# Optimization experiments

Measured on AMD Instinct MI355X. Metric: run time of the kernel, lower is better.

Reference implementation:

```python
import jax, jax.numpy as jnp
import numpy as np

NUM_ENT = 50000
NUM_REL2 = 474   # num_relations * 2
E = 400000
D = 100          # embedding / hidden dim (hardcoded in module)
B = 4            # num_bases
NEG_SLOPE = 0.2  # PyG RGATConv default


def setup_inputs() -> dict:
    key = jax.random.key(0)
    ks = jax.random.split(key, 8)
    inp = {
        "entity": jnp.arange(NUM_ENT, dtype=jnp.int32),
        "edge_index": jax.random.randint(ks[0], (2, E), 0, NUM_ENT),
        "edge_type": jax.random.randint(ks[1], (E,), 0, NUM_REL2),
        "edge_norm": jax.random.normal(ks[2], (E,), dtype=jnp.float32),
        "emb": jax.random.normal(ks[3], (NUM_ENT, D), dtype=jnp.float32),
    }
    scale = 1.0 / np.sqrt(D).astype(np.float32)
    for i, p in enumerate(("1", "2")):
        k = jax.random.split(ks[4 + i], 4)
        inp["basis" + p] = jax.random.normal(k[0], (B, D, D), dtype=jnp.float32) * scale
        inp["att" + p] = jax.random.normal(k[1], (NUM_REL2, B), dtype=jnp.float32) * 0.5
        inp["q" + p] = jax.random.normal(k[2], (D, 1), dtype=jnp.float32) * scale
        inp["k" + p] = jax.random.normal(k[3], (D, 1), dtype=jnp.float32) * scale
        inp["bias" + p] = jnp.zeros((D,), jnp.float32)
    return inp


def segment_softmax(scores, seg, num_segments):
    # numerically stable softmax over edges grouped by destination node
    m = jax.ops.segment_max(scores, seg, num_segments=num_segments)
    ex = jnp.exp(scores - m[seg])
    s = jax.ops.segment_sum(ex, seg, num_segments=num_segments)
    return ex / (s[seg] + 1e-16)


def rgat_conv(x, src, dst, etype, basis, att, q, k, bias, num_nodes):
    # basis decomposition: per-relation weight W_r = sum_b att[r,b] * basis[b]
    # computed implicitly: project x through each basis once, mix per-edge.
    xb = jnp.einsum('ni,bio->nbo', x, basis)          # [N, B, D]
    att_e = att[etype]                                # [E, B]
    hj = jnp.einsum('eb,ebo->eo', att_e, xb[src])     # transformed source feats [E, D]
    xq = jnp.einsum('nbo,oh->nb', xb, q)              # per-node, per-basis q-score [N, B]
    xk = jnp.einsum('nbo,oh->nb', xb, k)
    q_e = jnp.sum(att_e * xq[dst], axis=1)            # [E]
    k_e = jnp.sum(att_e * xk[src], axis=1)            # [E]
    alpha = jax.nn.leaky_relu(q_e + k_e, NEG_SLOPE)   # additive self-attention
    alpha = segment_softmax(alpha, dst, num_nodes)    # across-relation softmax per dst
    out = jax.ops.segment_sum(alpha[:, None] * hj, dst, num_segments=num_nodes)
    return out + bias


def reference(entity, edge_index, edge_type, edge_norm, emb,
              basis1, att1, q1, k1, bias1,
              basis2, att2, q2, k2, bias2):
    src, dst = edge_index[0], edge_index[1]
    n = entity.shape[0]
    x = emb[entity]                                   # [N, 100]
    x = jax.nn.relu(rgat_conv(x, src, dst, edge_type, basis1, att1, q1, k1, bias1, n))
    # dropout is identity in eval mode
    x = rgat_conv(x, src, dst, edge_type, basis2, att2, q2, k2, bias2, n)
    return x
```

## Files before the change

### kernel.cpp

```cpp
#include <hip/hip_runtime.h>

constexpr int N = 50000;
constexpr int E = 400000;
constexpr int D = 100;
constexpr int B = 4;
constexpr float NEG_SLOPE = 0.2f;

constexpr int SCAN_CHUNK = 2048;
constexpr int NB_SCAN = (N + SCAN_CHUNK - 1) / SCAN_CHUNK;
constexpr int CAP = 128;


__global__ void k_hist(const int* __restrict__ dst, int* __restrict__ deg) {
  int i = blockIdx.x * blockDim.x + threadIdx.x;
  int stride = gridDim.x * blockDim.x;
  for (; i < E; i += stride) atomicAdd(&deg[dst[i]], 1);
}

__global__ void k_scan1(const int* __restrict__ deg, int* __restrict__ incl,
                        int* __restrict__ bsums) {
  __shared__ int lds[256];
  int tid = threadIdx.x;
  int base = blockIdx.x * SCAN_CHUNK + tid * 8;
  int v[8]; int s = 0;
#pragma unroll
  for (int j = 0; j < 8; ++j) {
    int idx = base + j;
    int x = (idx < N) ? deg[idx] : 0;
    v[j] = x; s += x;
  }
  lds[tid] = s; __syncthreads();
  for (int off = 1; off < 256; off <<= 1) {
    int t = (tid >= off) ? lds[tid - off] : 0;
    __syncthreads();
    lds[tid] += t;
    __syncthreads();
  }
  int run = lds[tid] - s;
#pragma unroll
  for (int j = 0; j < 8; ++j) {
    int idx = base + j;
    run += v[j];
    if (idx < N) incl[idx] = run;
  }
  if (tid == 255) bsums[blockIdx.x] = lds[255];
}

__global__ void k_scan2(int* __restrict__ bsums, int nb) {
  if (threadIdx.x == 0 && blockIdx.x == 0) {
    int run = 0;
    for (int i = 0; i < nb; ++i) { int t = bsums[i]; bsums[i] = run; run += t; }
  }
}

__global__ void k_scan3(const int* __restrict__ incl, const int* __restrict__ bsums,
                        int* __restrict__ offs) {
  int i = blockIdx.x * blockDim.x + threadIdx.x;
  int stride = gridDim.x * blockDim.x;
  for (; i < N; i += stride) {
    offs[i + 1] = incl[i] + bsums[i / SCAN_CHUNK];
    if (i == 0) offs[0] = 0;
  }
}

__global__ void k_scatter(const int* __restrict__ srcArr, const int* __restrict__ dst,
                          const int* __restrict__ etype, const int* __restrict__ offs,
                          int* __restrict__ cursor, int* __restrict__ ssorted,
                          int* __restrict__ esorted) {
  int i = blockIdx.x * blockDim.x + threadIdx.x;
  int stride = gridDim.x * blockDim.x;
  for (; i < E; i += stride) {
    int d = dst[i];
    int pos = offs[d] + atomicAdd(&cursor[d], 1);
    ssorted[pos] = srcArr[i];
    esorted[pos] = etype[i];
  }
}

__global__ void k_gather(const float* __restrict__ emb, const int* __restrict__ entity,
                         float* __restrict__ X) {
  int idx = blockIdx.x * blockDim.x + threadIdx.x;
  int total = N * (D / 4);
  int stride = gridDim.x * blockDim.x;
  for (; idx < total; idx += stride) {
    int n = idx / (D / 4), c = idx % (D / 4);
    int r = entity[n];
    *(float4*)(X + (size_t)n * D + c * 4) = *(const float4*)(emb + (size_t)r * D + c * 4);
  }
}


__global__ void k_qbkb(const float* __restrict__ basis, const float* __restrict__ qv,
                       const float* __restrict__ kv, float* __restrict__ qb,
                       float* __restrict__ kb) {
  int t = blockIdx.x * blockDim.x + threadIdx.x;
  if (t < B * D) {
    const float* row = basis + t * D;
    float sq = 0.f, sk = 0.f;
    for (int o = 0; o < D; ++o) { float r = row[o]; sq += r * qv[o]; sk += r * kv[o]; }
    qb[t] = sq; kb[t] = sk;
  }
}

__global__ __launch_bounds__(256) void k_xqxk(
    const float* __restrict__ X, const float* __restrict__ qb,
    const float* __restrict__ kb, float* __restrict__ xq, float* __restrict__ xk) {
  __shared__ float qb_s[B * D], kb_s[B * D];
  int tid = threadIdx.x;
  for (int i = tid; i < B * D; i += 256) { qb_s[i] = qb[i]; kb_s[i] = kb[i]; }
  __syncthreads();
  int n = blockIdx.x * 256 + tid;
  if (n >= N) return;
  const float* x = X + (size_t)n * D;
  float aq[B] = {}, ak[B] = {};
  for (int i = 0; i < D; i += 4) {
    float4 xv = *(const float4*)(x + i);
#pragma unroll
    for (int b = 0; b < B; ++b) {
      float4 qv = *(const float4*)&qb_s[b * D + i];
      float4 kv = *(const float4*)&kb_s[b * D + i];
      aq[b] += xv.x * qv.x + xv.y * qv.y + xv.z * qv.z + xv.w * qv.w;
      ak[b] += xv.x * kv.x + xv.y * kv.y + xv.z * kv.z + xv.w * kv.w;
    }
  }
  *(float4*)(xq + (size_t)n * 4) = make_float4(aq[0], aq[1], aq[2], aq[3]);
  *(float4*)(xk + (size_t)n * 4) = make_float4(ak[0], ak[1], ak[2], ak[3]);
}

__device__ __forceinline__ float edge_score_p(int s, int et,
                                              const float* __restrict__ att,
                                              const float4 xq4,
                                              const float* __restrict__ xk,
                                              float4* a_out) {
  float4 a = *(const float4*)(att + et * 4);
  float4 xs = *(const float4*)(xk + s * 4);
  float qe = a.x * xq4.x + a.y * xq4.y + a.z * xq4.z + a.w * xq4.w;
  float ke = a.x * xs.x + a.y * xs.y + a.z * xs.z + a.w * xs.w;
  float sc = qe + ke;
  *a_out = a;
  return sc >= 0.f ? sc : NEG_SLOPE * sc;
}

__global__ __launch_bounds__(128) void k_node(
    const float* __restrict__ feat, const int* __restrict__ ssorted,
    const int* __restrict__ esorted, const float* __restrict__ att,
    const float* __restrict__ xq, const float* __restrict__ xk,
    const int* __restrict__ offs, float* __restrict__ agg) {
  int n = blockIdx.x;
  int tid = threadIdx.x;
  int lane = tid & 63, wid = tid >> 6;
  int o0 = offs[n], o1 = offs[n + 1];
  int deg = o1 - o0;
  float4 xq4 = *(const float4*)(xq + (size_t)n * 4);
  __shared__ float red[2];
  __shared__ float sc[CAP];
  __shared__ float4 a4[CAP];
  __shared__ int sbuf[CAP];

  if (deg <= CAP) {
    for (int i = tid; i < deg; i += 128) {
      int s = ssorted[o0 + i];
      int et = esorted[o0 + i];
      float4 a;
      float v = edge_score_p(s, et, att, xq4, xk, &a);
      sc[i] = v; a4[i] = a; sbuf[i] = s;
    }
    __syncthreads();
    float lm = -3.4e38f;
    for (int i = tid; i < deg; i += 128) lm = fmaxf(lm, sc[i]);
#pragma unroll
    for (int off = 32; off >= 1; off >>= 1) lm = fmaxf(lm, __shfl_xor(lm, off));
    if (lane == 0) red[wid] = lm;
    __syncthreads();
    float m = fmaxf(red[0], red[1]);
    __syncthreads();
    float ls = 0.f;
    for (int i = tid; i < deg; i += 128) {
      float ex = __expf(sc[i] - m);
      sc[i] = ex;
      ls += ex;
    }
#pragma unroll
    for (int off = 32; off >= 1; off >>= 1) ls += __shfl_xor(ls, off);
    if (lane == 0) red[wid] = ls;
    __syncthreads();
    float inv = 1.f / (red[0] + red[1] + 1e-16f);
    for (int i = tid; i < deg; i += 128) {
      float p = sc[i] * inv;
      float4 a = a4[i];
      a.x *= p; a.y *= p; a.z *= p; a.w *= p;
      a4[i] = a;
    }
    __syncthreads();
    if (tid < D) {
      float acc0 = 0.f, acc1 = 0.f, acc2 = 0.f, acc3 = 0.f;
      int i = 0;
      for (; i + 1 < deg; i += 2) {
        float4 aA = a4[i];     int sA = sbuf[i];
        float4 aB = a4[i + 1]; int sB = sbuf[i + 1];
        float xA = feat[(size_t)sA * D + tid];
        float xB = feat[(size_t)sB * D + tid];
        acc0 += aA.x * xA + aB.x * xB;
        acc1 += aA.y * xA + aB.y * xB;
        acc2 += aA.z * xA + aB.z * xB;
        acc3 += aA.w * xA + aB.w * xB;
      }
      if (i < deg) {
        float4 a = a4[i]; int s = sbuf[i];
        float xv = feat[(size_t)s * D + tid];
        acc0 += a.x * xv; acc1 += a.y * xv; acc2 += a.z * xv; acc3 += a.w * xv;
      }
      float* ag = agg + (size_t)n * (B * D) + tid;
      ag[0 * D] = acc0; ag[1 * D] = acc1; ag[2 * D] = acc2; ag[3 * D] = acc3;
    }
  } else {
    float lm = -3.4e38f;
    for (int i = tid; i < deg; i += 128) {
      float4 a;
      lm = fmaxf(lm, edge_score_p(ssorted[o0 + i], esorted[o0 + i], att, xq4, xk, &a));
    }
#pragma unroll
    for (int off = 32; off >= 1; off >>= 1) lm = fmaxf(lm, __shfl_xor(lm, off));
    if (lane == 0) red[wid] = lm;
    __syncthreads();
    float m = fmaxf(red[0], red[1]);
    __syncthreads();
    float ls = 0.f;
    for (int i = tid; i < deg; i += 128) {
      float4 a;
      ls += __expf(edge_score_p(ssorted[o0 + i], esorted[o0 + i], att, xq4, xk, &a) - m);
    }
#pragma unroll
    for (int off = 32; off >= 1; off >>= 1) ls += __shfl_xor(ls, off);
    if (lane == 0) red[wid] = ls;
    __syncthreads();
    float inv = 1.f / (red[0] + red[1] + 1e-16f);
    if (tid < D) {
      float acc0 = 0.f, acc1 = 0.f, acc2 = 0.f, acc3 = 0.f;
      for (int i = 0; i < deg; ++i) {
        int s = ssorted[o0 + i];
        float4 a;
        float v = edge_score_p(s, esorted[o0 + i], att, xq4, xk, &a);
        float p = __expf(v - m) * inv;
        float xv = feat[(size_t)s * D + tid];
        acc0 += p * a.x * xv;
        acc1 += p * a.y * xv;
        acc2 += p * a.z * xv;
        acc3 += p * a.w * xv;
      }
      float* ag = agg + (size_t)n * (B * D) + tid;
      ag[0 * D] = acc0; ag[1 * D] = acc1; ag[2 * D] = acc2; ag[3 * D] = acc3;
    }
  }
}

template <bool RELU>
__global__ __launch_bounds__(256) void k_gemm(const float* __restrict__ A,
                                              const float* __restrict__ W,
                                              const float* __restrict__ bias,
                                              float* __restrict__ out) {
  __shared__ float A_lds[64][36];
  __shared__ float W_lds[32][128];
  int tid = threadIdx.x;
  int nblk = blockIdx.x * 64;
  int o_lo = (tid & 15) * 4;
  int n_base = (tid >> 4) * 4;
  float acc[4][8] = {};
  for (int kc = 0; kc < 400; kc += 32) {
#pragma unroll
    for (int j = 0; j < 2; ++j) {
      int idx = tid + j * 256;
      int n_l = idx >> 3;
      int k4 = (idx & 7) * 4;
      int gn = nblk + n_l;
      float4 av = make_float4(0.f, 0.f, 0.f, 0.f);
      if (gn < N && kc + k4 + 3 < 400) av = *(const float4*)(A + (size_t)gn * 400 + kc + k4);
      *(float4*)&A_lds[n_l][k4] = av;
    }
#pragma unroll
    for (int j = 0; j < 4; ++j) {
      int idx = tid + j * 256;
      int k = idx >> 5;
      int o4 = (idx & 31) * 4;
      float4 v = make_float4(0.f, 0.f, 0.f, 0.f);
      if (o4 < D && kc + k < 400) v = *(const float4*)(W + (size_t)(kc + k) * D + o4);
      *(float4*)&W_lds[k][o4] = v;
    }
    __syncthreads();
#pragma unroll 4
    for (int k = 0; k < 32; ++k) {
      float4 w0 = *(const float4*)&W_lds[k][o_lo];
      float4 w1 = *(const float4*)&W_lds[k][o_lo + 64];
      float w[8] = {w0.x, w0.y, w0.z, w0.w, w1.x, w1.y, w1.z, w1.w};
#pragma unroll
      for (int i = 0; i < 4; ++i) {
        float a = A_lds[n_base + i][k];
#pragma unroll
        for (int jj = 0; jj < 8; ++jj) acc[i][jj] += a * w[jj];
      }
    }
    __syncthreads();
  }
  bool hi_ok = (o_lo + 64 < D - 3);
  float4 b0 = *(const float4*)(bias + o_lo);
  float4 b1 = hi_ok ? *(const float4*)(bias + o_lo + 64) : make_float4(0, 0, 0, 0);
#pragma unroll
  for (int i = 0; i < 4; ++i) {
    int gn = nblk + n_base + i;
    if (gn < N) {
      float4 r0, r1;
      r0.x = acc[i][0] + b0.x; r0.y = acc[i][1] + b0.y;
      r0.z = acc[i][2] + b0.z; r0.w = acc[i][3] + b0.w;
      r1.x = acc[i][4] + b1.x; r1.y = acc[i][5] + b1.y;
      r1.z = acc[i][6] + b1.z; r1.w = acc[i][7] + b1.w;
      if (RELU) {
        r0.x = fmaxf(r0.x, 0.f); r0.y = fmaxf(r0.y, 0.f);
        r0.z = fmaxf(r0.z, 0.f); r0.w = fmaxf(r0.w, 0.f);
        r1.x = fmaxf(r1.x, 0.f); r1.y = fmaxf(r1.y, 0.f);
        r1.z = fmaxf(r1.z, 0.f); r1.w = fmaxf(r1.w, 0.f);
      }
      *(float4*)(out + (size_t)gn * D + o_lo) = r0;
      if (hi_ok) *(float4*)(out + (size_t)gn * D + o_lo + 64) = r1;
    }
  }
}


extern "C" void kernel_launch(void* const* d_in, const int* in_sizes, int n_in,
                              void* d_out, int out_size, void* d_ws, size_t ws_size,
                              hipStream_t stream) {
  const int* entity = (const int*)d_in[0];
  const int* edge_index = (const int*)d_in[1];
  const int* etype = (const int*)d_in[2];
  const float* emb = (const float*)d_in[4];
  const float* basis1 = (const float*)d_in[5];
  const float* att1 = (const float*)d_in[6];
  const float* q1 = (const float*)d_in[7];
  const float* k1 = (const float*)d_in[8];
  const float* bias1 = (const float*)d_in[9];
  const float* basis2 = (const float*)d_in[10];
  const float* att2 = (const float*)d_in[11];
  const float* q2 = (const float*)d_in[12];
  const float* k2 = (const float*)d_in[13];
  const float* bias2 = (const float*)d_in[14];
  float* out = (float*)d_out;

  const int* srcArr = edge_index;
  const int* dstArr = edge_index + E;

  float* ws = (float*)d_ws;
  float* agg = ws;
  float* X1 = agg + (size_t)N * B * D;
  float* xq = X1 + (size_t)N * D;
  float* xk = xq + (size_t)N * B;
  float* qb = xk + (size_t)N * B;
  float* kb = qb + B * D;
  int* ssorted = (int*)(kb + B * D);
  int* esorted = ssorted + E;
  int* offs = esorted + E;
  int* deg = offs + (N + 1);
  int* cursor = deg + N;
  int* incl = cursor + N;
  int* bsums = incl + N;

  hipMemsetAsync(deg, 0, N * sizeof(int), stream);
  hipMemsetAsync(cursor, 0, N * sizeof(int), stream);
  k_hist<<<512, 256, 0, stream>>>(dstArr, deg);
  k_scan1<<<NB_SCAN, 256, 0, stream>>>(deg, incl, bsums);
  k_scan2<<<1, 64, 0, stream>>>(bsums, NB_SCAN);
  k_scan3<<<256, 256, 0, stream>>>(incl, bsums, offs);
  k_scatter<<<512, 256, 0, stream>>>(srcArr, dstArr, etype, offs, cursor, ssorted, esorted);
  k_gather<<<1024, 256, 0, stream>>>(emb, entity, X1);

  k_qbkb<<<2, 256, 0, stream>>>(basis1, q1, k1, qb, kb);
  k_xqxk<<<(N + 255) / 256, 256, 0, stream>>>(X1, qb, kb, xq, xk);
  k_node<<<N, 128, 0, stream>>>(X1, ssorted, esorted, att1, xq, xk, offs, agg);
  k_gemm<true><<<(N + 63) / 64, 256, 0, stream>>>(agg, basis1, bias1, out);

  k_qbkb<<<2, 256, 0, stream>>>(basis2, q2, k2, qb, kb);
  k_xqxk<<<(N + 255) / 256, 256, 0, stream>>>(out, qb, kb, xq, xk);
  k_node<<<N, 128, 0, stream>>>(out, ssorted, esorted, att2, xq, xk, offs, agg);
  k_gemm<false><<<(N + 63) / 64, 256, 0, stream>>>(agg, basis2, bias2, out);
}
```

Before: 484.6 us.

## Prefetch next GEMM K-chunk into registers and widen chunk to 64

The dense GEMM now stages a 64-wide K chunk instead of 32. It prefetches the next chunk's A and W tiles into registers while computing on the current LDS tile, which hides global load latency behind FMAs and halves the number of barrier rounds. In exchange it uses more registers and roughly double the LDS, which may lower occupancy. Seven 64-wide chunks cover K=400, with zero padding past 400.

```diff
diff --git a/kernel.cpp b/kernel.cpp
--- a/kernel.cpp
+++ b/kernel.cpp
@@ -259,36 +259,59 @@
                                               const float* __restrict__ W,
                                               const float* __restrict__ bias,
                                               float* __restrict__ out) {
-  __shared__ float A_lds[64][36];
-  __shared__ float W_lds[32][128];
+  __shared__ float A_lds[64][68];
+  __shared__ float W_lds[64][128];
   int tid = threadIdx.x;
   int nblk = blockIdx.x * 64;
   int o_lo = (tid & 15) * 4;
   int n_base = (tid >> 4) * 4;
   float acc[4][8] = {};
-  for (int kc = 0; kc < 400; kc += 32) {
-#pragma unroll
-    for (int j = 0; j < 2; ++j) {
-      int idx = tid + j * 256;
-      int n_l = idx >> 3;
-      int k4 = (idx & 7) * 4;
-      int gn = nblk + n_l;
-      float4 av = make_float4(0.f, 0.f, 0.f, 0.f);
-      if (gn < N && kc + k4 + 3 < 400) av = *(const float4*)(A + (size_t)gn * 400 + kc + k4);
-      *(float4*)&A_lds[n_l][k4] = av;
-    }
+
+  int a_n[4], a_k4[4];
+  int w_k[8], w_o4[8];
+#pragma unroll
+  for (int j = 0; j < 4; ++j) {
+    int idx = tid + j * 256;
+    a_n[j] = idx >> 4;
+    a_k4[j] = (idx & 15) * 4;
+  }
+#pragma unroll
+  for (int j = 0; j < 8; ++j) {
+    int idx = tid + j * 256;
+    w_k[j] = idx >> 5;
+    w_o4[j] = (idx & 31) * 4;
+  }
+
+  float4 a_reg[4], w_reg[8];
+  auto load_chunk = [&](int kc) {
 #pragma unroll
     for (int j = 0; j < 4; ++j) {
-      int idx = tid + j * 256;
-      int k = idx >> 5;
-      int o4 = (idx & 31) * 4;
-      float4 v = make_float4(0.f, 0.f, 0.f, 0.f);
-      if (o4 < D && kc + k < 400) v = *(const float4*)(W + (size_t)(kc + k) * D + o4);
-      *(float4*)&W_lds[k][o4] = v;
-    }
-    __syncthreads();
+      int gn = nblk + a_n[j];
+      int k = kc + a_k4[j];
+      a_reg[j] = (gn < N && k + 3 < 400) ? *(const float4*)(A + (size_t)gn * 400 + k)
+                                         : make_float4(0.f, 0.f, 0.f, 0.f);
+    }
+#pragma unroll
+    for (int j = 0; j < 8; ++j) {
+      int k = kc + w_k[j];
+      w_reg[j] = (w_o4[j] < D && k < 400)
+                     ? *(const float4*)(W + (size_t)k * D + w_o4[j])
+                     : make_float4(0.f, 0.f, 0.f, 0.f);
+    }
+  };
+
+  load_chunk(0);
+  constexpr int NC = 7;
+  for (int c = 0; c < NC; ++c) {
+    __syncthreads();
+#pragma unroll
+    for (int j = 0; j < 4; ++j) *(float4*)&A_lds[a_n[j]][a_k4[j]] = a_reg[j];
+#pragma unroll
+    for (int j = 0; j < 8; ++j) *(float4*)&W_lds[w_k[j]][w_o4[j]] = w_reg[j];
+    __syncthreads();
+    if (c + 1 < NC) load_chunk((c + 1) * 64);
 #pragma unroll 4
-    for (int k = 0; k < 32; ++k) {
+    for (int k = 0; k < 64; ++k) {
       float4 w0 = *(const float4*)&W_lds[k][o_lo];
       float4 w1 = *(const float4*)&W_lds[k][o_lo + 64];
       float w[8] = {w0.x, w0.y, w0.z, w0.w, w1.x, w1.y, w1.z, w1.w};
@@ -299,7 +322,6 @@
         for (int jj = 0; jj < 8; ++jj) acc[i][jj] += a * w[jj];
       }
     }
-    __syncthreads();
   }
   bool hi_ok = (o_lo + 64 < D - 3);
   float4 b0 = *(const float4*)(bias + o_lo);
```

Measured after the change: 485.8 us. Within noise of the previous version (+0.2%).

## Restructure GEMM tiling so each lane owns a row and waves split output columns

Applied to the files above, without the earlier changes.

Reworks the dense aggregation GEMM (N x 400 times 400 x 100). Each thread now handles one node row with 24-28 output columns, where each wave covers a slice of the 100 outputs. A is transposed into LDS so every lane reads its own A value, and W is read from LDS as wave-uniform broadcasts. K tiles grow from 32 to 64 and the 128-wide padded W tile is dropped to avoid wasted columns. The trade-off is more registers per thread and uneven work between waves, since wave 0 handles 28 columns and the others 24.

```diff
diff --git a/kernel.cpp b/kernel.cpp
--- a/kernel.cpp
+++ b/kernel.cpp
@@ -259,68 +259,85 @@
                                               const float* __restrict__ W,
                                               const float* __restrict__ bias,
                                               float* __restrict__ out) {
-  __shared__ float A_lds[64][36];
-  __shared__ float W_lds[32][128];
+  __shared__ float At[64][80];
+  __shared__ float Wf[64 * 100];
   int tid = threadIdx.x;
+  int lane = tid & 63;
+  int wv = tid >> 6;
   int nblk = blockIdx.x * 64;
-  int o_lo = (tid & 15) * 4;
-  int n_base = (tid >> 4) * 4;
-  float acc[4][8] = {};
-  for (int kc = 0; kc < 400; kc += 32) {
-#pragma unroll
-    for (int j = 0; j < 2; ++j) {
-      int idx = tid + j * 256;
-      int n_l = idx >> 3;
-      int k4 = (idx & 7) * 4;
-      int gn = nblk + n_l;
-      float4 av = make_float4(0.f, 0.f, 0.f, 0.f);
-      if (gn < N && kc + k4 + 3 < 400) av = *(const float4*)(A + (size_t)gn * 400 + kc + k4);
-      *(float4*)&A_lds[n_l][k4] = av;
-    }
-#pragma unroll
-    for (int j = 0; j < 4; ++j) {
-      int idx = tid + j * 256;
-      int k = idx >> 5;
-      int o4 = (idx & 31) * 4;
-      float4 v = make_float4(0.f, 0.f, 0.f, 0.f);
-      if (o4 < D && kc + k < 400) v = *(const float4*)(W + (size_t)(kc + k) * D + o4);
-      *(float4*)&W_lds[k][o4] = v;
-    }
-    __syncthreads();
-#pragma unroll 4
-    for (int k = 0; k < 32; ++k) {
-      float4 w0 = *(const float4*)&W_lds[k][o_lo];
-      float4 w1 = *(const float4*)&W_lds[k][o_lo + 64];
-      float w[8] = {w0.x, w0.y, w0.z, w0.w, w1.x, w1.y, w1.z, w1.w};
-#pragma unroll
-      for (int i = 0; i < 4; ++i) {
-        float a = A_lds[n_base + i][k];
-#pragma unroll
-        for (int jj = 0; jj < 8; ++jj) acc[i][jj] += a * w[jj];
-      }
-    }
-    __syncthreads();
-  }
-  bool hi_ok = (o_lo + 64 < D - 3);
-  float4 b0 = *(const float4*)(bias + o_lo);
-  float4 b1 = hi_ok ? *(const float4*)(bias + o_lo + 64) : make_float4(0, 0, 0, 0);
-#pragma unroll
-  for (int i = 0; i < 4; ++i) {
-    int gn = nblk + n_base + i;
-    if (gn < N) {
-      float4 r0, r1;
-      r0.x = acc[i][0] + b0.x; r0.y = acc[i][1] + b0.y;
-      r0.z = acc[i][2] + b0.z; r0.w = acc[i][3] + b0.w;
-      r1.x = acc[i][4] + b1.x; r1.y = acc[i][5] + b1.y;
-      r1.z = acc[i][6] + b1.z; r1.w = acc[i][7] + b1.w;
-      if (RELU) {
-        r0.x = fmaxf(r0.x, 0.f); r0.y = fmaxf(r0.y, 0.f);
-        r0.z = fmaxf(r0.z, 0.f); r0.w = fmaxf(r0.w, 0.f);
-        r1.x = fmaxf(r1.x, 0.f); r1.y = fmaxf(r1.y, 0.f);
-        r1.z = fmaxf(r1.z, 0.f); r1.w = fmaxf(r1.w, 0.f);
-      }
-      *(float4*)(out + (size_t)gn * D + o_lo) = r0;
-      if (hi_ok) *(float4*)(out + (size_t)gn * D + o_lo + 64) = r1;
+  int gn = nblk + lane;
+  int o_base = (wv == 0) ? 0 : 28 + (wv - 1) * 24;
+  float acc[28] = {};
+
+  int a_n = lane;
+  int a_kq = wv;
+  const float* arow = A + (size_t)(nblk + a_n) * 400;
+  bool arow_ok = (nblk + a_n) < N;
+
+  for (int kc = 0; kc < 400; kc += 64) {
+    __syncthreads();
+#pragma unroll
+    for (int j4 = 0; j4 < 4; ++j4) {
+      int k = kc + a_kq * 16 + j4 * 4;
+      float4 v = (arow_ok && k + 3 < 400) ? *(const float4*)(arow + k)
+                                          : make_float4(0.f, 0.f, 0.f, 0.f);
+      int kl = a_kq * 16 + j4 * 4;
+      At[kl + 0][a_n] = v.x;
+      At[kl + 1][a_n] = v.y;
+      At[kl + 2][a_n] = v.z;
+      At[kl + 3][a_n] = v.w;
+    }
+    for (int q = tid; q < 1600; q += 256) {
+      int w = q * 4;
+      int kl = w / 100;
+      int o = w - kl * 100;
+      int kg = kc + kl;
+      float4 v = (kg < 400) ? *(const float4*)(W + (size_t)kg * 100 + o)
+                            : make_float4(0.f, 0.f, 0.f, 0.f);
+      *(float4*)&Wf[w] = v;
+    }
+    __syncthreads();
+#pragma unroll 2
+    for (int k = 0; k < 64; ++k) {
+      float a = At[k][lane];
+      const float* wrow = &Wf[k * 100 + o_base];
+#pragma unroll
+      for (int q = 0; q < 6; ++q) {
+        float4 w4 = *(const float4*)(wrow + 4 * q);
+        acc[4 * q + 0] += a * w4.x;
+        acc[4 * q + 1] += a * w4.y;
+        acc[4 * q + 2] += a * w4.z;
+        acc[4 * q + 3] += a * w4.w;
+      }
+      if (wv == 0) {
+        float4 w4 = *(const float4*)(wrow + 24);
+        acc[24] += a * w4.x;
+        acc[25] += a * w4.y;
+        acc[26] += a * w4.z;
+        acc[27] += a * w4.w;
+      }
+    }
+  }
+  if (gn < N) {
+    int nq = (wv == 0) ? 7 : 6;
+    float* orow = out + (size_t)gn * 100 + o_base;
+    const float* brow = bias + o_base;
+#pragma unroll
+    for (int q = 0; q < 7; ++q) {
+      if (q < nq) {
+        float4 r;
+        r.x = acc[4 * q + 0] + brow[4 * q + 0];
+        r.y = acc[4 * q + 1] + brow[4 * q + 1];
+        r.z = acc[4 * q + 2] + brow[4 * q + 2];
+        r.w = acc[4 * q + 3] + brow[4 * q + 3];
+        if (RELU) {
+          r.x = fmaxf(r.x, 0.f);
+          r.y = fmaxf(r.y, 0.f);
+          r.z = fmaxf(r.z, 0.f);
+          r.w = fmaxf(r.w, 0.f);
+        }
+        *(float4*)(orow + 4 * q) = r;
+      }
     }
   }
 }
```

After: 643.7 us. 1.33x slower.

## Enlarge GEMM tile to 128 rows with transposed swizzled A in LDS

Applied to the files above, without the earlier changes.

Rewrites the node-by-basis GEMM so each block handles 128 rows with a K-chunk of 64, and each thread computes an 8x8 register tile instead of 4x8. A is stored transposed in LDS with an XOR swizzle, so each thread reads its 8 A values as two float4 loads instead of scalar loads. The goal is more FMAs per LDS read and fewer barriers. The costs are higher register pressure from 64 accumulators, fewer blocks (391) and larger LDS use, which may lower occupancy.

```diff
diff --git a/kernel.cpp b/kernel.cpp
--- a/kernel.cpp
+++ b/kernel.cpp
@@ -259,54 +259,66 @@
                                               const float* __restrict__ W,
                                               const float* __restrict__ bias,
                                               float* __restrict__ out) {
-  __shared__ float A_lds[64][36];
-  __shared__ float W_lds[32][128];
+  __shared__ float At[64 * 128];
+  __shared__ float Wf[64 * 128];
   int tid = threadIdx.x;
-  int nblk = blockIdx.x * 64;
-  int o_lo = (tid & 15) * 4;
-  int n_base = (tid >> 4) * 4;
-  float acc[4][8] = {};
-  for (int kc = 0; kc < 400; kc += 32) {
-#pragma unroll
-    for (int j = 0; j < 2; ++j) {
+  int o_g = tid & 15;
+  int n_g = tid >> 4;
+  int o_lo = o_g * 4;
+  int nblk = blockIdx.x * 128;
+  float acc[8][8] = {};
+
+  for (int kc = 0; kc < 400; kc += 64) {
+    __syncthreads();
+#pragma unroll
+    for (int j = 0; j < 8; ++j) {
       int idx = tid + j * 256;
-      int n_l = idx >> 3;
-      int k4 = (idx & 7) * 4;
-      int gn = nblk + n_l;
-      float4 av = make_float4(0.f, 0.f, 0.f, 0.f);
-      if (gn < N && kc + k4 + 3 < 400) av = *(const float4*)(A + (size_t)gn * 400 + kc + k4);
-      *(float4*)&A_lds[n_l][k4] = av;
-    }
-#pragma unroll
-    for (int j = 0; j < 4; ++j) {
+      int n_l = idx >> 4;
+      int k4 = (idx & 15) * 4;
+      int gn2 = nblk + n_l;
+      float4 v = (gn2 < N && kc + k4 + 3 < 400)
+                     ? *(const float4*)(A + (size_t)gn2 * 400 + kc + k4)
+                     : make_float4(0.f, 0.f, 0.f, 0.f);
+      int n8 = n_l >> 3, nlo = n_l & 7;
+#pragma unroll
+      for (int i = 0; i < 4; ++i) {
+        int k = k4 + i;
+        At[k * 128 + ((n8 ^ ((k >> 2) & 3)) << 3) + nlo] = (&v.x)[i];
+      }
+    }
+#pragma unroll
+    for (int j = 0; j < 8; ++j) {
       int idx = tid + j * 256;
-      int k = idx >> 5;
+      int kl = idx >> 5;
       int o4 = (idx & 31) * 4;
-      float4 v = make_float4(0.f, 0.f, 0.f, 0.f);
-      if (o4 < D && kc + k < 400) v = *(const float4*)(W + (size_t)(kc + k) * D + o4);
-      *(float4*)&W_lds[k][o4] = v;
+      int kg = kc + kl;
+      float4 v = (o4 < D && kg < 400)
+                     ? *(const float4*)(W + (size_t)kg * D + o4)
+                     : make_float4(0.f, 0.f, 0.f, 0.f);
+      *(float4*)&Wf[kl * 128 + o4] = v;
     }
     __syncthreads();
 #pragma unroll 4
-    for (int k = 0; k < 32; ++k) {
-      float4 w0 = *(const float4*)&W_lds[k][o_lo];
-      float4 w1 = *(const float4*)&W_lds[k][o_lo + 64];
-      float w[8] = {w0.x, w0.y, w0.z, w0.w, w1.x, w1.y, w1.z, w1.w};
-#pragma unroll
-      for (int i = 0; i < 4; ++i) {
-        float a = A_lds[n_base + i][k];
-#pragma unroll
-        for (int jj = 0; jj < 8; ++jj) acc[i][jj] += a * w[jj];
-      }
-    }
-    __syncthreads();
-  }
-  bool hi_ok = (o_lo + 64 < D - 3);
+    for (int k = 0; k < 64; ++k) {
+      int abase = k * 128 + ((n_g ^ ((k >> 2) & 3)) << 3);
+      float4 a0 = *(const float4*)&At[abase];
+      float4 a1 = *(const float4*)&At[abase + 4];
+      float4 w0 = *(const float4*)&Wf[k * 128 + o_lo];
+      float4 w1 = *(const float4*)&Wf[k * 128 + o_lo + 64];
+      float av[8] = {a0.x, a0.y, a0.z, a0.w, a1.x, a1.y, a1.z, a1.w};
+      float wv[8] = {w0.x, w0.y, w0.z, w0.w, w1.x, w1.y, w1.z, w1.w};
+#pragma unroll
+      for (int i = 0; i < 8; ++i)
+#pragma unroll
+        for (int jj = 0; jj < 8; ++jj) acc[i][jj] += av[i] * wv[jj];
+    }
+  }
+  bool hi_ok = (o_lo + 64 + 3) < D;
   float4 b0 = *(const float4*)(bias + o_lo);
   float4 b1 = hi_ok ? *(const float4*)(bias + o_lo + 64) : make_float4(0, 0, 0, 0);
 #pragma unroll
-  for (int i = 0; i < 4; ++i) {
-    int gn = nblk + n_base + i;
+  for (int i = 0; i < 8; ++i) {
+    int gn = nblk + n_g * 8 + i;
     if (gn < N) {
       float4 r0, r1;
       r0.x = acc[i][0] + b0.x; r0.y = acc[i][1] + b0.y;
@@ -375,10 +387,10 @@
   k_qbkb<<<2, 256, 0, stream>>>(basis1, q1, k1, qb, kb);
   k_xqxk<<<(N + 255) / 256, 256, 0, stream>>>(X1, qb, kb, xq, xk);
   k_node<<<N, 128, 0, stream>>>(X1, ssorted, esorted, att1, xq, xk, offs, agg);
-  k_gemm<true><<<(N + 63) / 64, 256, 0, stream>>>(agg, basis1, bias1, out);
+  k_gemm<true><<<(N + 127) / 128, 256, 0, stream>>>(agg, basis1, bias1, out);
 
   k_qbkb<<<2, 256, 0, stream>>>(basis2, q2, k2, qb, kb);
   k_xqxk<<<(N + 255) / 256, 256, 0, stream>>>(out, qb, kb, xq, xk);
   k_node<<<N, 128, 0, stream>>>(out, ssorted, esorted, att2, xq, xk, offs, agg);
-  k_gemm<false><<<(N + 63) / 64, 256, 0, stream>>>(agg, basis2, bias2, out);
-}
+  k_gemm<false><<<(N + 127) / 128, 256, 0, stream>>>(agg, basis2, bias2, out);
+}
```

Result: no change. 493.0 us (+1.7%).
